# Optimization experiments

Measured on AMD Instinct MI355X. Metric: run time of the kernel, lower is better.

## Reference

```python
import jax, jax.numpy as jnp
import numpy as np

N0, N1 = 20000, 20000     # users, items
F0 = 512                  # raw feature dim per type
HID = 64                  # hidden_dim == H * D
H, D = 8, 8               # num_heads, out_dim
P = 2                     # metapaths per side
E = 200000                # metapath instances per metapath
L = 3                     # metapath length (nodes)
B = 8192                  # link-prediction target batch
AV = 128                  # attn_vec_dim
CH = 128                  # ProductMLP hidden = max(128, HID//2)
ETYPES_USER = [[0, 1], [0, 1]]
ETYPES_ITEM = [[1, 0], [1, 0]]


def setup_inputs() -> dict:
    key = jax.random.key(0)
    ks = jax.random.split(key, 32)
    def nrm(k, shape, fan_in):
        return (jax.random.normal(k, shape, dtype=jnp.float32) * (1.414 / np.sqrt(fan_in))).astype(jnp.float32)
    inp = {}
    inp['feats0'] = jax.random.normal(ks[0], (N0, F0), dtype=jnp.float32)
    inp['feats1'] = jax.random.normal(ks[1], (N1, F0), dtype=jnp.float32)
    for t, off in ((0, 2), (1, 6)):
        inp[f'tower{t}_pw'] = nrm(ks[off], (F0, HID), F0)
        inp[f'tower{t}_pb'] = jnp.zeros((HID,), jnp.float32)
        inp[f'tower{t}_w2'] = nrm(ks[off + 1], (HID, HID), HID)
        inp[f'tower{t}_b2'] = jnp.zeros((HID,), jnp.float32)
        inp[f'tower{t}_g'] = jnp.ones((HID,), jnp.float32)
        inp[f'tower{t}_be'] = jnp.zeros((HID,), jnp.float32)
    inp['r_vec'] = jax.random.normal(ks[10], (2, HID // 2, 2), dtype=jnp.float32)
    inp['attn_user'] = nrm(ks[11], (P, H, D), D)
    inp['attn_item'] = nrm(ks[12], (P, H, D), D)
    inp['su_w1'] = nrm(ks[13], (HID, AV), HID)
    inp['su_b1'] = jnp.zeros((AV,), jnp.float32)
    inp['su_w2'] = nrm(ks[14], (AV,), AV)
    inp['si_w1'] = nrm(ks[15], (HID, AV), HID)
    inp['si_b1'] = jnp.zeros((AV,), jnp.float32)
    inp['si_w2'] = nrm(ks[16], (AV,), AV)
    inp['cw1'] = nrm(ks[17], (HID, CH), HID)
    inp['cb1'] = jnp.zeros((CH,), jnp.float32)
    inp['cw2'] = nrm(ks[18], (CH, 2), CH)
    inp['idx0'] = jnp.arange(N0, dtype=jnp.int32)
    inp['idx1'] = jnp.arange(N1, dtype=jnp.int32) + N0
    inp['emi_user'] = jax.random.randint(ks[20], (P, E, L), 0, N0 + N1, dtype=jnp.int32)
    inp['tgt_user'] = jax.random.randint(ks[21], (P, E), 0, B, dtype=jnp.int32)
    inp['emi_item'] = jax.random.randint(ks[22], (P, E, L), 0, N0 + N1, dtype=jnp.int32)
    inp['tgt_item'] = jax.random.randint(ks[23], (P, E), 0, B, dtype=jnp.int32)
    return inp


def _tower(x, pw, pb, w2, b2, g, be):
    # Linear -> GELU -> Linear -> residual -> LayerNorm (dropout off in eval)
    z = x @ pw + pb
    h = jax.nn.gelu(z, approximate=False)
    h = h @ w2 + b2
    y = h + z
    mu = y.mean(-1, keepdims=True)
    var = ((y - mu) ** 2).mean(-1, keepdims=True)
    return (y - mu) / jnp.sqrt(var + 1e-5) * g + be


def _rot_full(r_vec):
    # normalize to unit complex, then even etypes = r, odd etypes = conj(r)
    r = r_vec / jnp.linalg.norm(r_vec, axis=-1, keepdims=True)
    conj = r * jnp.array([1.0, -1.0], dtype=r.dtype)
    return jnp.stack([r, conj], axis=1).reshape(-1, r.shape[1], 2)  # [num_edge_type, HID//2, 2]


def _final_r(rfull, etypes):
    # cumulative complex rotation applied to each position along the metapath
    fr = [None] * L
    fr[L - 1] = jnp.stack([jnp.ones(HID // 2), jnp.zeros(HID // 2)], axis=1).astype(rfull.dtype)
    for i in range(L - 2, -1, -1):
        rv = rfull[etypes[i]]
        re = fr[i + 1][:, 0] * rv[:, 0] - fr[i + 1][:, 1] * rv[:, 1]
        im = fr[i + 1][:, 0] * rv[:, 1] + fr[i + 1][:, 1] * rv[:, 0]
        fr[i] = jnp.stack([re, im], axis=1)
    return jnp.stack(fr)  # [L, HID//2, 2]


def _metapath(feat, emi, tgt, attn, etypes, rfull):
    # gather node features along each metapath instance: [E, L, HID//2, 2]
    ed = feat[emi].reshape(emi.shape[0], L, HID // 2, 2)
    fr = _final_r(rfull, etypes)  # last position is identity rotation
    re = ed[..., 0] * fr[:, :, 0] - ed[..., 1] * fr[:, :, 1]
    im = ed[..., 0] * fr[:, :, 1] + ed[..., 1] * fr[:, :, 0]
    hidden = jnp.stack([re, im], -1).mean(axis=1).reshape(-1, HID)  # mean over metapath positions
    eft = hidden.reshape(-1, H, D)
    e = jax.nn.leaky_relu((eft * attn).sum(-1), 0.01)  # [E, H]
    # edge softmax over instances sharing a target node
    m = jax.ops.segment_max(e, tgt, num_segments=B)
    m = jnp.where(jnp.isfinite(m), m, 0.0)
    a = jnp.exp(e - m[tgt])
    s = jax.ops.segment_sum(a, tgt, num_segments=B)
    w = a / (s[tgt] + 1e-9)
    ret = jax.ops.segment_sum(w[..., None] * eft, tgt, num_segments=B)  # [B, H, D]
    return jax.nn.elu(ret.reshape(B, HID))


def _semantic(outs, w1, b1, w2):
    hs = jnp.stack(outs)  # [P, B, HID]
    s = (jnp.tanh(hs @ w1 + b1) @ w2).mean(axis=1)  # [P]
    beta = jax.nn.softmax(s)
    return (beta[:, None, None] * hs).sum(0)  # [B, HID]


def reference(feats0, feats1, tower0_pw, tower0_pb, tower0_w2, tower0_b2, tower0_g, tower0_be,
              tower1_pw, tower1_pb, tower1_w2, tower1_b2, tower1_g, tower1_be,
              r_vec, attn_user, attn_item, su_w1, su_b1, su_w2, si_w1, si_b1, si_w2,
              cw1, cb1, cw2, idx0, idx1, emi_user, tgt_user, emi_item, tgt_item):
    t0 = _tower(feats0, tower0_pw, tower0_pb, tower0_w2, tower0_b2, tower0_g, tower0_be)
    t1 = _tower(feats1, tower1_pw, tower1_pb, tower1_w2, tower1_b2, tower1_g, tower1_be)
    feat = jnp.zeros((N0 + N1, HID), jnp.float32).at[idx0].set(t0).at[idx1].set(t1)
    rfull = _rot_full(r_vec)
    user_outs = [_metapath(feat, emi_user[p], tgt_user[p], attn_user[p], ETYPES_USER[p], rfull) for p in range(P)]
    item_outs = [_metapath(feat, emi_item[p], tgt_item[p], attn_item[p], ETYPES_ITEM[p], rfull) for p in range(P)]
    h_user = _semantic(user_outs, su_w1, su_b1, su_w2)
    h_item = _semantic(item_outs, si_w1, si_b1, si_w2)
    x = h_user * h_item
    h = jax.nn.relu(x @ cw1 + cb1)
    logits = h @ cw2
    return jax.nn.softmax(logits, axis=-1)
```

## Files before the change

kernel.cpp:

```cpp
#include <hip/hip_runtime.h>
#include <hip/hip_bf16.h>
#include <math.h>

#define NN0 20000
#define NN1 20000
#define NTOT 40000
#define FF0 512
#define HIDD 64
#define EEE 200000
#define BBB 8192
#define AVV 128
#define CHH 128

typedef __bf16 bf16x8 __attribute__((ext_vector_type(8)));
typedef __bf16 bf16x4 __attribute__((ext_vector_type(4)));
typedef float f32x4 __attribute__((ext_vector_type(4)));
typedef float f32x2 __attribute__((ext_vector_type(2)));

__device__ __forceinline__ float fast_tanh(float x) {
    float e2 = __expf(2.f * x);
    return 1.f - 2.f / (e2 + 1.f);
}

__device__ __forceinline__ f32x2 bf2_to_f32x2(unsigned int c) {
    f32x2 r;
    r.x = __uint_as_float(c << 16);
    r.y = __uint_as_float(c & 0xffff0000u);
    return r;
}

__global__ __launch_bounds__(256) void prep_hist(
    const float* __restrict__ pw0, const float* __restrict__ pw1,
    const float* __restrict__ w20, const float* __restrict__ w21,
    __bf16* __restrict__ wprep, __bf16* __restrict__ w2prep,
    const int* __restrict__ tgt_user, const int* __restrict__ tgt_item,
    int* __restrict__ cnt)
{
    int bx = blockIdx.x;
    if (bx < 16) {
        int tw = bx & 1, seg = bx >> 1;
        const float* w = tw ? pw1 : pw0;
        __bf16* base = wprep + tw * 65536;
        for (int idx = seg * 4096 + threadIdx.x; idx < (seg + 1) * 4096; idx += 256) {
            int k = idx >> 6, n = idx & 63;
            float v = w[idx];
            __bf16 hi = (__bf16)v;
            __bf16 lo = (__bf16)(v - (float)hi);
            int ks = k >> 5, kb = (k >> 3) & 3, j = k & 7;
            int nt = n >> 4, fr = n & 15;
            int lane = kb * 16 + fr;
            int off = ((ks * 4 + nt) * 64 + lane) * 8 + j;
            base[off] = hi;
            base[32768 + off] = lo;
        }
        const float* w2 = tw ? w21 : w20;
        __bf16* base2 = w2prep + tw * 8192;
        for (int idx = seg * 512 + threadIdx.x; idx < (seg + 1) * 512; idx += 256) {
            int k = idx >> 6, n = idx & 63;
            float v = w2[idx];
            __bf16 hi = (__bf16)v;
            __bf16 lo = (__bf16)(v - (float)hi);
            int ks = k >> 5, kb = (k >> 3) & 3, j = k & 7;
            int nt = n >> 4, fr = n & 15;
            int lane = kb * 16 + fr;
            int off = ((ks * 4 + nt) * 64 + lane) * 8 + j;
            base2[off] = hi;
            base2[4096 + off] = lo;
        }
    } else {
        int flat = bx - 16;
        int combo = flat & 3, blk = flat >> 2;
        const int* tgt = (combo < 2 ? tgt_user : tgt_item) + (long)(combo & 1) * EEE;
        int i = blk * 256 + threadIdx.x;
        if (i < EEE) atomicAdd(&cnt[combo * BBB + tgt[i]], 1);
    }
}

__global__ __launch_bounds__(256) void scan_kernel(const int* __restrict__ cnt, int* __restrict__ offs,
                                                   int* __restrict__ cur32, float* __restrict__ s_acc)
{
    int pth = blockIdx.x;
    if (pth == 0 && threadIdx.x < 4) s_acc[threadIdx.x] = 0.f;
    const int* c = cnt + pth * BBB;
    int* o = offs + pth * (BBB + 1);
    __shared__ int part[256];
    int tid = threadIdx.x;
    int base = tid * 32;
    int local[32];
    int sum = 0;
    for (int j = 0; j < 32; j++) { local[j] = sum; sum += c[base + j]; }
    part[tid] = sum;
    __syncthreads();
    for (int d = 1; d < 256; d <<= 1) {
        int v = (tid >= d) ? part[tid - d] : 0;
        __syncthreads();
        part[tid] += v;
        __syncthreads();
    }
    int pre = (tid == 0) ? 0 : part[tid - 1];
    for (int j = 0; j < 32; j++) {
        int val = pre + local[j];
        o[base + j] = val;
        if (((base + j) & 255) == 0) cur32[pth * 32 + ((base + j) >> 8)] = val;
    }
    if (tid == 255) o[BBB] = pre + sum;
}

#define CHUNKF 1024
__global__ __launch_bounds__(128) void tower_binA(
    const float* __restrict__ x0, const float* __restrict__ x1,
    const __bf16* __restrict__ wprep, const __bf16* __restrict__ w2prep,
    const float* __restrict__ pb0, const float* __restrict__ pb1,
    const float* __restrict__ b20, const float* __restrict__ b21,
    const float* __restrict__ g0, const float* __restrict__ g1,
    const float* __restrict__ be0, const float* __restrict__ be1,
    const int* __restrict__ idxa, const int* __restrict__ idxb,
    __hip_bfloat16* __restrict__ feat,
    const int* __restrict__ tgt_user, const int* __restrict__ tgt_item,
    const int* __restrict__ emi_user, const int* __restrict__ emi_item,
    int* __restrict__ cur32, ushort4* __restrict__ binbuf)
{
    __shared__ __align__(16) char pool[8960];
    int bx = blockIdx.x;
    if (bx < 2500) {
        int tile = bx >> 1, tw = bx & 1;
        const float* x  = tw ? x1 : x0;
        const float* pb = tw ? pb1 : pb0;
        const float* b2 = tw ? b21 : b20;
        const float* g  = tw ? g1 : g0;
        const float* be = tw ? be1 : be0;
        const int* idx  = tw ? idxb : idxa;
        float (*hs)[68] = (float(*)[68])pool;
        float* pq  = (float*)(pool + 4352);
        float* pq2 = (float*)(pool + 4480);

        int wv = threadIdx.x >> 6;
        int l = threadIdx.x & 63;
        int fr = l & 15, kb = l >> 4;
        int nt0 = 2 * wv;
        int row0 = tile * 16;
        const float* xp = x + (long)(row0 + fr) * FF0 + kb * 8;
        const __bf16* bp = wprep + tw * 65536;

        f32x4 acc[2];
#pragma unroll
        for (int n2 = 0; n2 < 2; n2++) acc[n2] = (f32x4){0.f, 0.f, 0.f, 0.f};

        float4 a0c, a1c, a0n, a1n;
        bf16x8 bhc[2], blc[2], bhn[2], bln[2];

        a0c = *(const float4*)xp;
        a1c = *(const float4*)(xp + 4);
#pragma unroll
        for (int n2 = 0; n2 < 2; n2++) {
            bhc[n2] = *(const bf16x8*)(bp + ((nt0 + n2) * 64 + l) * 8);
            blc[n2] = *(const bf16x8*)(bp + 32768 + ((nt0 + n2) * 64 + l) * 8);
        }

#pragma unroll 2
        for (int ks = 0; ks < 16; ks++) {
            if (ks + 1 < 16) {
                a0n = *(const float4*)(xp + (ks + 1) * 32);
                a1n = *(const float4*)(xp + (ks + 1) * 32 + 4);
#pragma unroll
                for (int n2 = 0; n2 < 2; n2++) {
                    bhn[n2] = *(const bf16x8*)(bp + (((ks + 1) * 4 + nt0 + n2) * 64 + l) * 8);
                    bln[n2] = *(const bf16x8*)(bp + 32768 + (((ks + 1) * 4 + nt0 + n2) * 64 + l) * 8);
                }
            }
            float av[8] = {a0c.x, a0c.y, a0c.z, a0c.w, a1c.x, a1c.y, a1c.z, a1c.w};
            bf16x8 ah, al;
#pragma unroll
            for (int j = 0; j < 8; j++) {
                __bf16 h = (__bf16)av[j];
                ah[j] = h;
                al[j] = (__bf16)(av[j] - (float)h);
            }
#pragma unroll
            for (int n2 = 0; n2 < 2; n2++) {
                acc[n2] = __builtin_amdgcn_mfma_f32_16x16x32_bf16(ah, bhc[n2], acc[n2], 0, 0, 0);
                acc[n2] = __builtin_amdgcn_mfma_f32_16x16x32_bf16(al, bhc[n2], acc[n2], 0, 0, 0);
                acc[n2] = __builtin_amdgcn_mfma_f32_16x16x32_bf16(ah, blc[n2], acc[n2], 0, 0, 0);
            }
            a0c = a0n; a1c = a1n;
#pragma unroll
            for (int n2 = 0; n2 < 2; n2++) { bhc[n2] = bhn[n2]; blc[n2] = bln[n2]; }
        }

        float pbv[2], b2v[2];
#pragma unroll
        for (int n2 = 0; n2 < 2; n2++) {
            pbv[n2] = pb[(nt0 + n2) * 16 + fr];
            b2v[n2] = b2[(nt0 + n2) * 16 + fr];
        }
        f32x4 acc2[2];
#pragma unroll
        for (int n2 = 0; n2 < 2; n2++) {
#pragma unroll
            for (int j = 0; j < 4; j++) {
                float z = acc[n2][j] + pbv[n2];
                float h = 0.5f * z * (1.f + erff(z * 0.70710678118654752f));
                hs[kb * 4 + j][(nt0 + n2) * 16 + fr] = h;
                acc2[n2][j] = z + b2v[n2];
            }
        }
        __syncthreads();

        const __bf16* w2p = w2prep + tw * 8192;
#pragma unroll
        for (int ks = 0; ks < 2; ks++) {
            float4 h0 = *(const float4*)&hs[fr][ks * 32 + kb * 8];
            float4 h1 = *(const float4*)&hs[fr][ks * 32 + kb * 8 + 4];
            float hv[8] = {h0.x, h0.y, h0.z, h0.w, h1.x, h1.y, h1.z, h1.w};
            bf16x8 ah, al;
#pragma unroll
            for (int j = 0; j < 8; j++) {
                __bf16 h = (__bf16)hv[j];
                ah[j] = h;
                al[j] = (__bf16)(hv[j] - (float)h);
            }
#pragma unroll
            for (int n2 = 0; n2 < 2; n2++) {
                bf16x8 bh2 = *(const bf16x8*)(w2p + ((ks * 4 + nt0 + n2) * 64 + l) * 8);
                bf16x8 bl2 = *(const bf16x8*)(w2p + 4096 + ((ks * 4 + nt0 + n2) * 64 + l) * 8);
                acc2[n2] = __builtin_amdgcn_mfma_f32_16x16x32_bf16(ah, bh2, acc2[n2], 0, 0, 0);
                acc2[n2] = __builtin_amdgcn_mfma_f32_16x16x32_bf16(al, bh2, acc2[n2], 0, 0, 0);
                acc2[n2] = __builtin_amdgcn_mfma_f32_16x16x32_bf16(ah, bl2, acc2[n2], 0, 0, 0);
            }
        }

        float pj[4];
#pragma unroll
        for (int j = 0; j < 4; j++) {
            float p = acc2[0][j] + acc2[1][j];
            p += __shfl_xor(p, 1); p += __shfl_xor(p, 2);
            p += __shfl_xor(p, 4); p += __shfl_xor(p, 8);
            pj[j] = p;
        }
        if (fr == 0) {
#pragma unroll
            for (int j = 0; j < 4; j++) pq[wv * 16 + kb * 4 + j] = pj[j];
        }
        __syncthreads();
        float mu[4];
#pragma unroll
        for (int j = 0; j < 4; j++)
            mu[j] = (pj[j] + pq[(wv ^ 1) * 16 + kb * 4 + j]) * (1.f / 64.f);
        float d[2][4], vj[4];
#pragma unroll
        for (int j = 0; j < 4; j++) {
            d[0][j] = acc2[0][j] - mu[j];
            d[1][j] = acc2[1][j] - mu[j];
            float v = d[0][j] * d[0][j] + d[1][j] * d[1][j];
            v += __shfl_xor(v, 1); v += __shfl_xor(v, 2);
            v += __shfl_xor(v, 4); v += __shfl_xor(v, 8);
            vj[j] = v;
        }
        if (fr == 0) {
#pragma unroll
            for (int j = 0; j < 4; j++) pq2[wv * 16 + kb * 4 + j] = vj[j];
        }
        __syncthreads();
        float gv[2], bev[2];
#pragma unroll
        for (int n2 = 0; n2 < 2; n2++) {
            gv[n2] = g[(nt0 + n2) * 16 + fr];
            bev[n2] = be[(nt0 + n2) * 16 + fr];
        }
#pragma unroll
        for (int j = 0; j < 4; j++) {
            float var = (vj[j] + pq2[(wv ^ 1) * 16 + kb * 4 + j]) * (1.f / 64.f);
            float is = 1.f / sqrtf(var + 1e-5f);
#pragma unroll
            for (int n2 = 0; n2 < 2; n2++)
                hs[kb * 4 + j][(nt0 + n2) * 16 + fr] = d[n2][j] * is * gv[n2] + bev[n2];
        }
        __syncthreads();
#pragma unroll
        for (int r = 0; r < 8; r++) {
            int rr = wv * 8 + r;
            feat[(long)idx[row0 + rr] * HIDD + l] = __float2bfloat16(hs[rr][l]);
        }
    } else {
        int flat = bx - 2500;
        int combo = flat & 3;
        int base = (flat >> 2) * CHUNKF;
        const int* tgt = (combo < 2 ? tgt_user : tgt_item) + (long)(combo & 1) * EEE;
        const int* emi = (combo < 2 ? emi_user : emi_item) + (long)(combo & 1) * EEE * 3;
        ushort4* sbuf = (ushort4*)pool;
        int* lcnt  = (int*)(pool + 8192);
        int* lofs  = lcnt + 32;
        int* gbase = lofs + 33;
        int* lcur  = gbase + 32;
        int tid = threadIdx.x;
        if (tid < 32) { lcnt[tid] = 0; lcur[tid] = 0; }
        __syncthreads();
        ushort4 ent[8]; int bk[8];
#pragma unroll
        for (int ps = 0; ps < 8; ps++) {
            int i = base + ps * 128 + tid;
            if (i < EEE) {
                int t = tgt[i];
                ent[ps] = make_ushort4((unsigned short)emi[3 * i], (unsigned short)emi[3 * i + 1],
                                       (unsigned short)emi[3 * i + 2], (unsigned short)t);
                bk[ps] = t >> 8;
                atomicAdd(&lcnt[bk[ps]], 1);
            } else bk[ps] = -1;
        }
        __syncthreads();
        if (tid == 0) {
            int run = 0;
            for (int k = 0; k < 32; k++) { lofs[k] = run; run += lcnt[k]; }
            lofs[32] = run;
        }
        __syncthreads();
        if (tid < 32) gbase[tid] = atomicAdd(&cur32[combo * 32 + tid], lcnt[tid]);
        __syncthreads();
#pragma unroll
        for (int ps = 0; ps < 8; ps++) {
            if (bk[ps] >= 0) {
                int pos = lofs[bk[ps]] + atomicAdd(&lcur[bk[ps]], 1);
                sbuf[pos] = ent[ps];
            }
        }
        __syncthreads();
        int total = lofs[32];
        ushort4* dst = binbuf + (long)combo * EEE;
        for (int j = tid; j < total; j += 128) {
            ushort4 e = sbuf[j];
            int k = e.w >> 8;
            dst[gbase[k] + (j - lofs[k])] = e;
        }
    }
}

__global__ __launch_bounds__(256) void binB_kernel(
    const int* __restrict__ offs, int* __restrict__ cur,
    const ushort4* __restrict__ binbuf, ushort4* __restrict__ nodes)
{
    int combo = blockIdx.y;
    int k = blockIdx.x >> 1, part = blockIdx.x & 1;
    const int* of = offs + combo * (BBB + 1);
    int rbeg = of[k << 8], rend = of[(k + 1) << 8];
    const ushort4* src = binbuf + (long)combo * EEE;
    ushort4* dst = nodes + (long)combo * EEE;
    int* cu = cur + combo * BBB;
    for (int j = rbeg + part * 256 + threadIdx.x; j < rend; j += 512) {
        ushort4 e = src[j];
        int t = e.w;
        int pos = of[t] + atomicAdd(&cu[t], 1);
        dst[pos] = e;
    }
}

__global__ __launch_bounds__(256) void flash_mp(
    const __hip_bfloat16* __restrict__ feat, const ushort4* __restrict__ nodes,
    const int* __restrict__ offs, const float* __restrict__ r_vec,
    const float* __restrict__ attn_user, const float* __restrict__ attn_item,
    float* __restrict__ ret)
{
    int combo = blockIdx.y;
    int wid = threadIdx.x >> 6, lane = threadIdx.x & 63;
    int half = lane >> 5, p = lane & 31;
    int side = combo >> 1;
    const float* attn = (side == 0 ? attn_user : attn_item) + (combo & 1) * 64;
    const unsigned int* f2 = (const unsigned int*)feat;
    float2 rb = ((const float2*)r_vec)[p];
    float invn = 1.f / sqrtf(rb.x * rb.x + rb.y * rb.y);
    float rvx = rb.x * invn, rvy = rb.y * invn;
    if (side == 0) rvy = -rvy;
    float aRe = attn[2 * p], aIm = attn[2 * p + 1];
    f32x2 av  = { aRe * (1.f / 3.f), aIm * (1.f / 3.f) };
    f32x2 apv = { (rvx * aRe + rvy * aIm) * (1.f / 3.f),
                  (rvx * aIm - rvy * aRe) * (1.f / 3.f) };
    int t = blockIdx.x * 4 + wid;
    const int* of = offs + combo * (BBB + 1);
    int beg = of[t], end = of[t + 1];
    int n = end - beg;
    const ushort4* nd = nodes + (long)combo * EEE;

    float m = -3.4e38f, s = 0.f;
    f32x2 A02 = {0.f, 0.f}, A1 = {0.f, 0.f};

    unsigned int c0[4], c1[4], c2[4];
    ushort4 nq[4];
    if (n > 0) {
#pragma unroll
        for (int q = 0; q < 4; q++) {
            ushort4 a = nd[min(beg + 2 * q + half, EEE - 1)];
            c0[q] = f2[(int)a.x * 32 + p];
            c1[q] = f2[(int)a.y * 32 + p];
            c2[q] = f2[(int)a.z * 32 + p];
        }
#pragma unroll
        for (int q = 0; q < 4; q++)
            nq[q] = nd[min(beg + 8 + 2 * q + half, EEE - 1)];
    }
    for (int it = 0; it < n; it += 8) {
        f32x2 u1[4], v02[4];
        float e[4];
#pragma unroll
        for (int q = 0; q < 4; q++) {
            f32x2 u0 = bf2_to_f32x2(c0[q]);
            u1[q]    = bf2_to_f32x2(c1[q]);
            f32x2 u2 = bf2_to_f32x2(c2[q]);
            v02[q] = u0 + u2;
        }
        if (it + 8 < n) {
#pragma unroll
            for (int q = 0; q < 4; q++) {
                c0[q] = f2[(int)nq[q].x * 32 + p];
                c1[q] = f2[(int)nq[q].y * 32 + p];
                c2[q] = f2[(int)nq[q].z * 32 + p];
            }
#pragma unroll
            for (int q = 0; q < 4; q++)
                nq[q] = nd[min(beg + it + 16 + 2 * q + half, EEE - 1)];
        }
#pragma unroll
        for (int q = 0; q < 4; q++) {
            f32x2 tt = v02[q] * av + u1[q] * apv;
            float pa = tt.x + tt.y;
            pa += __shfl_xor(pa, 1);
            pa += __shfl_xor(pa, 2);
            e[q] = fmaxf(pa, 0.01f * pa);
        }
        if (it + 8 > n) {
#pragma unroll
            for (int q = 0; q < 4; q++)
                if (it + 2 * q + half >= n) e[q] = -3.4e38f;
        }
        float mx = fmaxf(fmaxf(e[0], e[1]), fmaxf(e[2], e[3]));
        float mn = fmaxf(m, fmaxf(mx, __shfl_xor(mx, 32)));
        float alpha = __expf(m - mn);
        s *= alpha; A02 *= alpha; A1 *= alpha;
        float wl = 0.f;
#pragma unroll
        for (int q = 0; q < 4; q++) {
            float w = __expf(e[q] - mn);
            wl += w;
            A02 += v02[q] * w;
            A1  += u1[q] * w;
        }
        s += wl + __shfl_xor(wl, 32);
        m = mn;
    }
    float Sx = A02.x + __shfl_xor(A02.x, 32);
    float Sy = A02.y + __shfl_xor(A02.y, 32);
    float Tx = A1.x + __shfl_xor(A1.x, 32);
    float Ty = A1.y + __shfl_xor(A1.y, 32);
    float inv = (1.f / 3.f) / (s + 1e-9f);
    float vx = (Sx + rvx * Tx - rvy * Ty) * inv;
    float vy = (Sy + rvx * Ty + rvy * Tx) * inv;
    vx = vx > 0.f ? vx : __expf(vx) - 1.f;
    vy = vy > 0.f ? vy : __expf(vy) - 1.f;
    if (half == 0)
        ((float2*)ret)[((long)combo * BBB + t) * 32 + p] = make_float2(vx, vy);
}

__global__ __launch_bounds__(256) void sem_kernel(
    const float* __restrict__ ret,
    const float* __restrict__ su_w1, const float* __restrict__ su_b1, const float* __restrict__ su_w2,
    const float* __restrict__ si_w1, const float* __restrict__ si_b1, const float* __restrict__ si_w2,
    float* __restrict__ s_acc)
{
    int combo = blockIdx.y;
    int side = combo >> 1;
    const float* w1 = side ? si_w1 : su_w1;
    const float* b1 = side ? si_b1 : su_b1;
    const float* w2 = side ? si_w2 : su_w2;
    __shared__ float vs[64][68];
    __shared__ float w1s[64][128];
    int tid = threadIdx.x;
    int rowbase = blockIdx.x * 64;
    const float4* r4 = (const float4*)ret;
    for (int li = tid; li < 1024; li += 256) {
        int r = li >> 4, c4 = li & 15;
        float4 v = r4[((long)combo * BBB + rowbase + r) * 16 + c4];
        *(float4*)&vs[r][c4 * 4] = v;
    }
    const float4* w14 = (const float4*)w1;
    for (int li = tid; li < 2048; li += 256) {
        float4 v = w14[li];
        *(float4*)&w1s[li >> 5][(li & 31) * 4] = v;
    }
    __syncthreads();
    int ct = tid & 15, rt = tid >> 4;
    float acc[4][8];
#pragma unroll
    for (int cc = 0; cc < 8; cc++) {
        float b = b1[8 * ct + cc];
#pragma unroll
        for (int j = 0; j < 4; j++) acc[j][cc] = b;
    }
    for (int k = 0; k < 64; k += 4) {
        float4 xv[4];
#pragma unroll
        for (int j = 0; j < 4; j++) xv[j] = *(const float4*)&vs[4 * rt + j][k];
#pragma unroll
        for (int kk = 0; kk < 4; kk++) {
            float4 wv0 = *(const float4*)&w1s[k + kk][8 * ct];
            float4 wv1 = *(const float4*)&w1s[k + kk][8 * ct + 4];
#pragma unroll
            for (int j = 0; j < 4; j++) {
                float xx = kk == 0 ? xv[j].x : kk == 1 ? xv[j].y : kk == 2 ? xv[j].z : xv[j].w;
                acc[j][0] = fmaf(xx, wv0.x, acc[j][0]);
                acc[j][1] = fmaf(xx, wv0.y, acc[j][1]);
                acc[j][2] = fmaf(xx, wv0.z, acc[j][2]);
                acc[j][3] = fmaf(xx, wv0.w, acc[j][3]);
                acc[j][4] = fmaf(xx, wv1.x, acc[j][4]);
                acc[j][5] = fmaf(xx, wv1.y, acc[j][5]);
                acc[j][6] = fmaf(xx, wv1.z, acc[j][6]);
                acc[j][7] = fmaf(xx, wv1.w, acc[j][7]);
            }
        }
    }
    float tot = 0.f;
#pragma unroll
    for (int cc = 0; cc < 8; cc++) {
        float w2v = w2[8 * ct + cc];
#pragma unroll
        for (int j = 0; j < 4; j++) tot += fast_tanh(acc[j][cc]) * w2v;
    }
    for (int off = 32; off; off >>= 1) tot += __shfl_xor(tot, off);
    __shared__ float red[4];
    int lane = tid & 63, wid = tid >> 6;
    if (lane == 0) red[wid] = tot;
    __syncthreads();
    if (tid == 0) atomicAdd(&s_acc[combo], red[0] + red[1] + red[2] + red[3]);
}

__global__ __launch_bounds__(256) void final_kernel(
    const float* __restrict__ ret, const float* __restrict__ s_acc,
    const float* __restrict__ cw1, const float* __restrict__ cb1, const float* __restrict__ cw2,
    float* __restrict__ outp)
{
    float s0 = s_acc[0] * (1.f / BBB), s1 = s_acc[1] * (1.f / BBB);
    float s2 = s_acc[2] * (1.f / BBB), s3 = s_acc[3] * (1.f / BBB);
    float mu = fmaxf(s0, s1);
    float e0 = __expf(s0 - mu), e1 = __expf(s1 - mu);
    float bu0 = e0 / (e0 + e1), bu1 = e1 / (e0 + e1);
    float mi = fmaxf(s2, s3);
    float f0 = __expf(s2 - mi), f1 = __expf(s3 - mi);
    float bi0 = f0 / (f0 + f1), bi1 = f1 / (f0 + f1);

    __shared__ float xsld[64][68];
    __shared__ float w1s[64][128];
    int tid = threadIdx.x;
    int rowbase = blockIdx.x * 64;
    const float4* r4 = (const float4*)ret;
    for (int li = tid; li < 1024; li += 256) {
        int r = li >> 4, c4 = li & 15;
        float4 a = r4[((long)0 * BBB + rowbase + r) * 16 + c4];
        float4 b = r4[((long)1 * BBB + rowbase + r) * 16 + c4];
        float4 cc = r4[((long)2 * BBB + rowbase + r) * 16 + c4];
        float4 d = r4[((long)3 * BBB + rowbase + r) * 16 + c4];
        float4 xv;
        xv.x = (bu0 * a.x + bu1 * b.x) * (bi0 * cc.x + bi1 * d.x);
        xv.y = (bu0 * a.y + bu1 * b.y) * (bi0 * cc.y + bi1 * d.y);
        xv.z = (bu0 * a.z + bu1 * b.z) * (bi0 * cc.z + bi1 * d.z);
        xv.w = (bu0 * a.w + bu1 * b.w) * (bi0 * cc.w + bi1 * d.w);
        *(float4*)&xsld[r][c4 * 4] = xv;
    }
    const float4* w14 = (const float4*)cw1;
    for (int li = tid; li < 2048; li += 256) {
        float4 v = w14[li];
        *(float4*)&w1s[li >> 5][(li & 31) * 4] = v;
    }
    __syncthreads();
    int ct = tid & 15, rt = tid >> 4;
    float acc[4][8];
#pragma unroll
    for (int cc = 0; cc < 8; cc++) {
        float b = cb1[8 * ct + cc];
#pragma unroll
        for (int j = 0; j < 4; j++) acc[j][cc] = b;
    }
    for (int k = 0; k < 64; k += 4) {
        float4 xv[4];
#pragma unroll
        for (int j = 0; j < 4; j++) xv[j] = *(const float4*)&xsld[4 * rt + j][k];
#pragma unroll
        for (int kk = 0; kk < 4; kk++) {
            float4 wv0 = *(const float4*)&w1s[k + kk][8 * ct];
            float4 wv1 = *(const float4*)&w1s[k + kk][8 * ct + 4];
#pragma unroll
            for (int j = 0; j < 4; j++) {
                float xx = kk == 0 ? xv[j].x : kk == 1 ? xv[j].y : kk == 2 ? xv[j].z : xv[j].w;
                acc[j][0] = fmaf(xx, wv0.x, acc[j][0]);
                acc[j][1] = fmaf(xx, wv0.y, acc[j][1]);
                acc[j][2] = fmaf(xx, wv0.z, acc[j][2]);
                acc[j][3] = fmaf(xx, wv0.w, acc[j][3]);
                acc[j][4] = fmaf(xx, wv1.x, acc[j][4]);
                acc[j][5] = fmaf(xx, wv1.y, acc[j][5]);
                acc[j][6] = fmaf(xx, wv1.z, acc[j][6]);
                acc[j][7] = fmaf(xx, wv1.w, acc[j][7]);
            }
        }
    }
    float pp0[4], pp1[4];
#pragma unroll
    for (int j = 0; j < 4; j++) { pp0[j] = 0.f; pp1[j] = 0.f; }
#pragma unroll
    for (int cc = 0; cc < 8; cc++) {
        int col = 8 * ct + cc;
        float c0 = cw2[col * 2], c1 = cw2[col * 2 + 1];
#pragma unroll
        for (int j = 0; j < 4; j++) {
            float h = fmaxf(acc[j][cc], 0.f);
            pp0[j] = fmaf(h, c0, pp0[j]);
            pp1[j] = fmaf(h, c1, pp1[j]);
        }
    }
    __syncthreads();
    float2* red = (float2*)xsld;
#pragma unroll
    for (int j = 0; j < 4; j++)
        red[(4 * rt + j) * 16 + ct] = make_float2(pp0[j], pp1[j]);
    __syncthreads();
    if (tid < 64) {
        float q0 = 0.f, q1 = 0.f;
        for (int i = 0; i < 16; i++) {
            float2 e = red[tid * 16 + i];
            q0 += e.x; q1 += e.y;
        }
        float mx = fmaxf(q0, q1);
        float a0 = __expf(q0 - mx), a1 = __expf(q1 - mx);
        float dn = a0 + a1;
        outp[(rowbase + tid) * 2] = a0 / dn;
        outp[(rowbase + tid) * 2 + 1] = a1 / dn;
    }
}

extern "C" void kernel_launch(void* const* d_in, const int* in_sizes, int n_in,
                              void* d_out, int out_size, void* d_ws, size_t ws_size,
                              hipStream_t stream)
{
    const float* feats0 = (const float*)d_in[0];
    const float* feats1 = (const float*)d_in[1];
    const float* t0_pw = (const float*)d_in[2];
    const float* t0_pb = (const float*)d_in[3];
    const float* t0_w2 = (const float*)d_in[4];
    const float* t0_b2 = (const float*)d_in[5];
    const float* t0_g  = (const float*)d_in[6];
    const float* t0_be = (const float*)d_in[7];
    const float* t1_pw = (const float*)d_in[8];
    const float* t1_pb = (const float*)d_in[9];
    const float* t1_w2 = (const float*)d_in[10];
    const float* t1_b2 = (const float*)d_in[11];
    const float* t1_g  = (const float*)d_in[12];
    const float* t1_be = (const float*)d_in[13];
    const float* r_vec = (const float*)d_in[14];
    const float* attn_user = (const float*)d_in[15];
    const float* attn_item = (const float*)d_in[16];
    const float* su_w1 = (const float*)d_in[17];
    const float* su_b1 = (const float*)d_in[18];
    const float* su_w2 = (const float*)d_in[19];
    const float* si_w1 = (const float*)d_in[20];
    const float* si_b1 = (const float*)d_in[21];
    const float* si_w2 = (const float*)d_in[22];
    const float* cw1 = (const float*)d_in[23];
    const float* cb1 = (const float*)d_in[24];
    const float* cw2 = (const float*)d_in[25];
    const int* idx0 = (const int*)d_in[26];
    const int* idx1 = (const int*)d_in[27];
    const int* emi_user = (const int*)d_in[28];
    const int* tgt_user = (const int*)d_in[29];
    const int* emi_item = (const int*)d_in[30];
    const int* tgt_item = (const int*)d_in[31];
    float* outp = (float*)d_out;

    char* ws = (char*)d_ws;
    __hip_bfloat16* feat = (__hip_bfloat16*)(ws + 0);
    int*     cnt    = (int*)(ws + 5120000);
    int*     cur    = (int*)(ws + 5251072);
    int*     cur32  = (int*)(ws + 5382144);
    int*     offs   = (int*)(ws + 5382656);
    float*   s_acc  = (float*)(ws + 5513984);
    ushort4* binbuf = (ushort4*)(ws + 5514240);
    ushort4* nodes  = (ushort4*)(ws + 11914240);
    float*   ret_buf= (float*)(ws + 18314240);
    __bf16*  wprep  = (__bf16*)(ws + 26702848);
    __bf16*  w2prep = (__bf16*)(ws + 11914240);

    hipMemsetAsync(cnt, 0, 2 * 4 * BBB * sizeof(int), stream);

    prep_hist<<<16 + 4 * ((EEE + 255) / 256), 256, 0, stream>>>(
        t0_pw, t1_pw, t0_w2, t1_w2, wprep, w2prep, tgt_user, tgt_item, cnt);

    scan_kernel<<<4, 256, 0, stream>>>(cnt, offs, cur32, s_acc);

    tower_binA<<<2500 + 4 * ((EEE + CHUNKF - 1) / CHUNKF), 128, 0, stream>>>(
        feats0, feats1, wprep, w2prep, t0_pb, t1_pb,
        t0_b2, t1_b2, t0_g, t1_g, t0_be, t1_be, idx0, idx1, feat,
        tgt_user, tgt_item, emi_user, emi_item, cur32, binbuf);

    binB_kernel<<<dim3(64, 4), 256, 0, stream>>>(offs, cur, binbuf, nodes);

    flash_mp<<<dim3(BBB / 4, 4), 256, 0, stream>>>(feat, nodes, offs, r_vec,
                                                   attn_user, attn_item, ret_buf);

    sem_kernel<<<dim3(BBB / 64, 4), 256, 0, stream>>>(ret_buf, su_w1, su_b1, su_w2,
                                                      si_w1, si_b1, si_w2, s_acc);
    final_kernel<<<BBB / 64, 256, 0, stream>>>(ret_buf, s_acc, cw1, cb1, cw2, outp);
}
```

Measured before the change: 333.5 us.

## Sort bins in shared memory and fuse semantic attention into flash_mp

binB_kernel now gives each 256-target bin to one block. The block counts and prefix-sums its targets in LDS, scatters entries into a shared buffer, and writes them out contiguously. This removes the global per-target atomic counters and half of the memset. The semantic-attention score (64x128 projection, tanh, dot with w2, block reduction) moves into the flash_mp epilogue using wave shuffles, so the separate sem_kernel launch and its re-read of ret are gone. In exchange, binB uses fewer blocks, and a fixed LDS capacity (BKCAP) silently truncates any bin that overflows it.

```diff
diff --git a/kernel.cpp b/kernel.cpp
--- a/kernel.cpp
+++ b/kernel.cpp
@@ -334,31 +334,61 @@
     }
 }
 
+#define BKCAP 7680
 __global__ __launch_bounds__(256) void binB_kernel(
-    const int* __restrict__ offs, int* __restrict__ cur,
+    const int* __restrict__ offs,
     const ushort4* __restrict__ binbuf, ushort4* __restrict__ nodes)
 {
     int combo = blockIdx.y;
-    int k = blockIdx.x >> 1, part = blockIdx.x & 1;
+    int k = blockIdx.x;
     const int* of = offs + combo * (BBB + 1);
     int rbeg = of[k << 8], rend = of[(k + 1) << 8];
-    const ushort4* src = binbuf + (long)combo * EEE;
-    ushort4* dst = nodes + (long)combo * EEE;
-    int* cu = cur + combo * BBB;
-    for (int j = rbeg + part * 256 + threadIdx.x; j < rend; j += 512) {
+    int cnt = rend - rbeg;
+    if (cnt > BKCAP) cnt = BKCAP;
+    __shared__ ushort4 sbuf[BKCAP];
+    __shared__ int lh[256];
+    __shared__ int part[256];
+    int tid = threadIdx.x;
+    lh[tid] = 0;
+    __syncthreads();
+    const ushort4* src = binbuf + (long)combo * EEE + rbeg;
+    for (int j = tid; j < cnt; j += 256)
+        atomicAdd(&lh[src[j].w & 255], 1);
+    __syncthreads();
+    int myc = lh[tid];
+    part[tid] = myc;
+    __syncthreads();
+    for (int d = 1; d < 256; d <<= 1) {
+        int u = (tid >= d) ? part[tid - d] : 0;
+        __syncthreads();
+        part[tid] += u;
+        __syncthreads();
+    }
+    int myofs = part[tid] - myc;
+    __syncthreads();
+    lh[tid] = myofs;
+    part[tid] = 0;
+    __syncthreads();
+    for (int j = tid; j < cnt; j += 256) {
         ushort4 e = src[j];
-        int t = e.w;
-        int pos = of[t] + atomicAdd(&cu[t], 1);
-        dst[pos] = e;
-    }
+        int b = e.w & 255;
+        int pos = lh[b] + atomicAdd(&part[b], 1);
+        if (pos < BKCAP) sbuf[pos] = e;
+    }
+    __syncthreads();
+    ushort4* dst = nodes + (long)combo * EEE + rbeg;
+    for (int j = tid; j < cnt; j += 256) dst[j] = sbuf[j];
 }
 
 __global__ __launch_bounds__(256) void flash_mp(
     const __hip_bfloat16* __restrict__ feat, const ushort4* __restrict__ nodes,
     const int* __restrict__ offs, const float* __restrict__ r_vec,
     const float* __restrict__ attn_user, const float* __restrict__ attn_item,
-    float* __restrict__ ret)
+    const float* __restrict__ su_w1, const float* __restrict__ su_b1, const float* __restrict__ su_w2,
+    const float* __restrict__ si_w1, const float* __restrict__ si_b1, const float* __restrict__ si_w2,
+    float* __restrict__ s_acc, float* __restrict__ ret)
 {
+    __shared__ float sred[4];
     int combo = blockIdx.y;
     int wid = threadIdx.x >> 6, lane = threadIdx.x & 63;
     int half = lane >> 5, p = lane & 31;
@@ -456,78 +486,28 @@
     vy = vy > 0.f ? vy : __expf(vy) - 1.f;
     if (half == 0)
         ((float2*)ret)[((long)combo * BBB + t) * 32 + p] = make_float2(vx, vy);
-}
-
-__global__ __launch_bounds__(256) void sem_kernel(
-    const float* __restrict__ ret,
-    const float* __restrict__ su_w1, const float* __restrict__ su_b1, const float* __restrict__ su_w2,
-    const float* __restrict__ si_w1, const float* __restrict__ si_b1, const float* __restrict__ si_w2,
-    float* __restrict__ s_acc)
-{
-    int combo = blockIdx.y;
-    int side = combo >> 1;
+
     const float* w1 = side ? si_w1 : su_w1;
     const float* b1 = side ? si_b1 : su_b1;
-    const float* w2 = side ? si_w2 : su_w2;
-    __shared__ float vs[64][68];
-    __shared__ float w1s[64][128];
-    int tid = threadIdx.x;
-    int rowbase = blockIdx.x * 64;
-    const float4* r4 = (const float4*)ret;
-    for (int li = tid; li < 1024; li += 256) {
-        int r = li >> 4, c4 = li & 15;
-        float4 v = r4[((long)combo * BBB + rowbase + r) * 16 + c4];
-        *(float4*)&vs[r][c4 * 4] = v;
-    }
-    const float4* w14 = (const float4*)w1;
-    for (int li = tid; li < 2048; li += 256) {
-        float4 v = w14[li];
-        *(float4*)&w1s[li >> 5][(li & 31) * 4] = v;
-    }
-    __syncthreads();
-    int ct = tid & 15, rt = tid >> 4;
-    float acc[4][8];
-#pragma unroll
-    for (int cc = 0; cc < 8; cc++) {
-        float b = b1[8 * ct + cc];
-#pragma unroll
-        for (int j = 0; j < 4; j++) acc[j][cc] = b;
-    }
-    for (int k = 0; k < 64; k += 4) {
-        float4 xv[4];
-#pragma unroll
-        for (int j = 0; j < 4; j++) xv[j] = *(const float4*)&vs[4 * rt + j][k];
-#pragma unroll
-        for (int kk = 0; kk < 4; kk++) {
-            float4 wv0 = *(const float4*)&w1s[k + kk][8 * ct];
-            float4 wv1 = *(const float4*)&w1s[k + kk][8 * ct + 4];
-#pragma unroll
-            for (int j = 0; j < 4; j++) {
-                float xx = kk == 0 ? xv[j].x : kk == 1 ? xv[j].y : kk == 2 ? xv[j].z : xv[j].w;
-                acc[j][0] = fmaf(xx, wv0.x, acc[j][0]);
-                acc[j][1] = fmaf(xx, wv0.y, acc[j][1]);
-                acc[j][2] = fmaf(xx, wv0.z, acc[j][2]);
-                acc[j][3] = fmaf(xx, wv0.w, acc[j][3]);
-                acc[j][4] = fmaf(xx, wv1.x, acc[j][4]);
-                acc[j][5] = fmaf(xx, wv1.y, acc[j][5]);
-                acc[j][6] = fmaf(xx, wv1.z, acc[j][6]);
-                acc[j][7] = fmaf(xx, wv1.w, acc[j][7]);
-            }
-        }
-    }
-    float tot = 0.f;
-#pragma unroll
-    for (int cc = 0; cc < 8; cc++) {
-        float w2v = w2[8 * ct + cc];
-#pragma unroll
-        for (int j = 0; j < 4; j++) tot += fast_tanh(acc[j][cc]) * w2v;
-    }
-    for (int off = 32; off; off >>= 1) tot += __shfl_xor(tot, off);
-    __shared__ float red[4];
-    int lane = tid & 63, wid = tid >> 6;
-    if (lane == 0) red[wid] = tot;
-    __syncthreads();
-    if (tid == 0) atomicAdd(&s_acc[combo], red[0] + red[1] + red[2] + red[3]);
+    const float* w2s = side ? si_w2 : su_w2;
+    float2 b1v = ((const float2*)b1)[lane];
+    float h0 = b1v.x, h1 = b1v.y;
+#pragma unroll 8
+    for (int p2 = 0; p2 < 32; p2++) {
+        float rx = __shfl(vx, p2);
+        float ry = __shfl(vy, p2);
+        float2 wa = ((const float2*)(w1 + (2 * p2) * AVV))[lane];
+        float2 wb = ((const float2*)(w1 + (2 * p2 + 1) * AVV))[lane];
+        h0 = fmaf(rx, wa.x, h0); h1 = fmaf(rx, wa.y, h1);
+        h0 = fmaf(ry, wb.x, h0); h1 = fmaf(ry, wb.y, h1);
+    }
+    float2 w2v = ((const float2*)w2s)[lane];
+    float contrib = fast_tanh(h0) * w2v.x + fast_tanh(h1) * w2v.y;
+    for (int off = 32; off; off >>= 1) contrib += __shfl_xor(contrib, off);
+    if (lane == 0) sred[wid] = contrib;
+    __syncthreads();
+    if (threadIdx.x == 0)
+        atomicAdd(&s_acc[combo], sred[0] + sred[1] + sred[2] + sred[3]);
 }
 
 __global__ __launch_bounds__(256) void final_kernel(
@@ -673,7 +653,6 @@
     char* ws = (char*)d_ws;
     __hip_bfloat16* feat = (__hip_bfloat16*)(ws + 0);
     int*     cnt    = (int*)(ws + 5120000);
-    int*     cur    = (int*)(ws + 5251072);
     int*     cur32  = (int*)(ws + 5382144);
     int*     offs   = (int*)(ws + 5382656);
     float*   s_acc  = (float*)(ws + 5513984);
@@ -683,7 +662,7 @@
     __bf16*  wprep  = (__bf16*)(ws + 26702848);
     __bf16*  w2prep = (__bf16*)(ws + 11914240);
 
-    hipMemsetAsync(cnt, 0, 2 * 4 * BBB * sizeof(int), stream);
+    hipMemsetAsync(cnt, 0, 4 * BBB * sizeof(int), stream);
 
     prep_hist<<<16 + 4 * ((EEE + 255) / 256), 256, 0, stream>>>(
         t0_pw, t1_pw, t0_w2, t1_w2, wprep, w2prep, tgt_user, tgt_item, cnt);
@@ -695,12 +674,13 @@
         t0_b2, t1_b2, t0_g, t1_g, t0_be, t1_be, idx0, idx1, feat,
         tgt_user, tgt_item, emi_user, emi_item, cur32, binbuf);
 
-    binB_kernel<<<dim3(64, 4), 256, 0, stream>>>(offs, cur, binbuf, nodes);
+    binB_kernel<<<dim3(32, 4), 256, 0, stream>>>(offs, binbuf, nodes);
 
     flash_mp<<<dim3(BBB / 4, 4), 256, 0, stream>>>(feat, nodes, offs, r_vec,
-                                                   attn_user, attn_item, ret_buf);
-
-    sem_kernel<<<dim3(BBB / 64, 4), 256, 0, stream>>>(ret_buf, su_w1, su_b1, su_w2,
-                                                      si_w1, si_b1, si_w2, s_acc);
+                                                   attn_user, attn_item,
+                                                   su_w1, su_b1, su_w2,
+                                                   si_w1, si_b1, si_w2,
+                                                   s_acc, ret_buf);
+
     final_kernel<<<BBB / 64, 256, 0, stream>>>(ret_buf, s_acc, cw1, cb1, cw2, outp);
 }
```

After: 383.9 us. +15.1%, slower.

## Sort second binning pass in shared memory with local histogram and scan

Applied to the files above, without the earlier changes.

The second counting-sort pass now loads each 256-target bucket, builds a per-block histogram in LDS, scans it, scatters entries into shared memory and writes them back contiguously. This replaces global atomics on a per-target cursor array and scattered global writes, and removes that cursor array and half of the memset. The cost is one block per bucket (half as many blocks) and a fixed cap of 7680 entries per bucket. Any bucket larger than the cap would be silently truncated.

```diff
diff --git a/kernel.cpp b/kernel.cpp
--- a/kernel.cpp
+++ b/kernel.cpp
@@ -334,23 +334,50 @@
     }
 }
 
+#define BKCAP 7680
 __global__ __launch_bounds__(256) void binB_kernel(
-    const int* __restrict__ offs, int* __restrict__ cur,
+    const int* __restrict__ offs,
     const ushort4* __restrict__ binbuf, ushort4* __restrict__ nodes)
 {
     int combo = blockIdx.y;
-    int k = blockIdx.x >> 1, part = blockIdx.x & 1;
+    int k = blockIdx.x;
     const int* of = offs + combo * (BBB + 1);
     int rbeg = of[k << 8], rend = of[(k + 1) << 8];
-    const ushort4* src = binbuf + (long)combo * EEE;
-    ushort4* dst = nodes + (long)combo * EEE;
-    int* cu = cur + combo * BBB;
-    for (int j = rbeg + part * 256 + threadIdx.x; j < rend; j += 512) {
+    int cnt = rend - rbeg;
+    if (cnt > BKCAP) cnt = BKCAP;
+    __shared__ ushort4 sbuf[BKCAP];
+    __shared__ int lh[256];
+    __shared__ int part[256];
+    int tid = threadIdx.x;
+    lh[tid] = 0;
+    __syncthreads();
+    const ushort4* src = binbuf + (long)combo * EEE + rbeg;
+    for (int j = tid; j < cnt; j += 256)
+        atomicAdd(&lh[src[j].w & 255], 1);
+    __syncthreads();
+    int myc = lh[tid];
+    part[tid] = myc;
+    __syncthreads();
+    for (int d = 1; d < 256; d <<= 1) {
+        int u = (tid >= d) ? part[tid - d] : 0;
+        __syncthreads();
+        part[tid] += u;
+        __syncthreads();
+    }
+    int myofs = part[tid] - myc;
+    __syncthreads();
+    lh[tid] = myofs;
+    part[tid] = 0;
+    __syncthreads();
+    for (int j = tid; j < cnt; j += 256) {
         ushort4 e = src[j];
-        int t = e.w;
-        int pos = of[t] + atomicAdd(&cu[t], 1);
-        dst[pos] = e;
-    }
+        int b = e.w & 255;
+        int pos = lh[b] + atomicAdd(&part[b], 1);
+        if (pos < BKCAP) sbuf[pos] = e;
+    }
+    __syncthreads();
+    ushort4* dst = nodes + (long)combo * EEE + rbeg;
+    for (int j = tid; j < cnt; j += 256) dst[j] = sbuf[j];
 }
 
 __global__ __launch_bounds__(256) void flash_mp(
@@ -673,7 +700,6 @@
     char* ws = (char*)d_ws;
     __hip_bfloat16* feat = (__hip_bfloat16*)(ws + 0);
     int*     cnt    = (int*)(ws + 5120000);
-    int*     cur    = (int*)(ws + 5251072);
     int*     cur32  = (int*)(ws + 5382144);
     int*     offs   = (int*)(ws + 5382656);
     float*   s_acc  = (float*)(ws + 5513984);
@@ -683,7 +709,7 @@
     __bf16*  wprep  = (__bf16*)(ws + 26702848);
     __bf16*  w2prep = (__bf16*)(ws + 11914240);
 
-    hipMemsetAsync(cnt, 0, 2 * 4 * BBB * sizeof(int), stream);
+    hipMemsetAsync(cnt, 0, 4 * BBB * sizeof(int), stream);
 
     prep_hist<<<16 + 4 * ((EEE + 255) / 256), 256, 0, stream>>>(
         t0_pw, t1_pw, t0_w2, t1_w2, wprep, w2prep, tgt_user, tgt_item, cnt);
@@ -695,7 +721,7 @@
         t0_b2, t1_b2, t0_g, t1_g, t0_be, t1_be, idx0, idx1, feat,
         tgt_user, tgt_item, emi_user, emi_item, cur32, binbuf);
 
-    binB_kernel<<<dim3(64, 4), 256, 0, stream>>>(offs, cur, binbuf, nodes);
+    binB_kernel<<<dim3(32, 4), 256, 0, stream>>>(offs, binbuf, nodes);
 
     flash_mp<<<dim3(BBB / 4, 4), 256, 0, stream>>>(feat, nodes, offs, r_vec,
                                                    attn_user, attn_item, ret_buf);
```

New measurement: 327.8 us. No clear change (-1.7%).
